# Kernel tuning notes

Measured on AMD Instinct MI355X. Metric: run time of the kernel, lower is better.

The kernel has to match this reference:

```python
import jax, jax.numpy as jnp
import numpy as np
from jax import lax

B, P, K = 16, 1024, 32          # clouds, points per cloud, kNN neighbors
N = B * P
NCLS = 40
DIMS = [3, 64, 128, 256]


def setup_inputs() -> dict:
    key = jax.random.key(0)
    ks = jax.random.split(key, 16)
    inp = {
        "x": jax.random.normal(ks[0], (N, DIMS[0]), dtype=jnp.float32),
        "batch": jnp.repeat(jnp.arange(B, dtype=jnp.int64), P),
        "target": jax.random.randint(ks[1], (N,), 0, NCLS, dtype=jnp.int64),
    }
    for i, (fi, fo) in enumerate(zip(DIMS[:-1], DIMS[1:])):
        scale = 1.0 / np.sqrt(2 * fi)
        inp[f"W{i+1}"] = jax.random.normal(ks[2 + 2 * i], (2 * fi, fo), dtype=jnp.float32) * scale
        inp[f"b{i+1}"] = jnp.zeros((fo,), dtype=jnp.float32)
    inp["Wc"] = jax.random.normal(ks[10], (DIMS[-1], NCLS), dtype=jnp.float32) * (1.0 / np.sqrt(DIMS[-1]))
    inp["bc"] = jnp.zeros((NCLS,), dtype=jnp.float32)
    return inp


def knn_graph(x):
    """Per-cloud kNN (loop=False). x: [N,F] with nodes grouped in B clouds of P.
    Returns global neighbor indices [N, K]."""
    xb = x.reshape(B, P, -1)
    sq = jnp.sum(xb * xb, axis=-1)                       # [B,P]
    d2 = sq[:, :, None] + sq[:, None, :] - 2.0 * jnp.einsum("bpf,bqf->bpq", xb, xb)
    d2 = d2 + jnp.eye(P, dtype=x.dtype) * jnp.finfo(x.dtype).max  # exclude self-loops
    _, idx = lax.top_k(-d2, K)                           # [B,P,K] local indices
    gidx = idx + (jnp.arange(B) * P)[:, None, None]      # local -> global node ids
    return gidx.reshape(N, K)


def edge_conv(x, nbr, W, b):
    """EdgeConv: max_j MLP([x_i, x_j - x_i])."""
    xj = x[nbr]                                          # [N,K,F] gather
    xi = x[:, None, :]
    feat = jnp.concatenate([jnp.broadcast_to(xi, xj.shape), xj - xi], axis=-1)  # [N,K,2F]
    h = jnp.einsum("nkf,fo->nko", feat, W) + b           # [N,K,F']
    return jnp.max(h, axis=1)                            # max aggregation


def reference(x, batch, target, W1, b1, W2, b2, W3, b3, Wc, bc):
    del batch  # structure encoded as B clouds of P contiguous nodes
    for W, b in ((W1, b1), (W2, b2), (W3, b3)):
        nbr = knn_graph(x)                               # dynamic graph per layer
        x = jax.nn.relu(edge_conv(x, nbr, W, b))
    logits = x @ Wc + bc                                 # [N, NCLS]
    probs = jax.nn.softmax(logits, axis=-1)
    logp = jax.nn.log_softmax(logits, axis=-1)           # == probs.log()
    loss = -jnp.mean(jnp.take_along_axis(logp, target[:, None], axis=-1))
    return loss, probs
```

## Files before the change

### kernel.cpp

```cpp
#include <hip/hip_runtime.h>
#include <float.h>
#include <math.h>

#define BCLOUDS 16
#define PPTS    1024
#define NPTS    (BCLOUDS * PPTS)
#define KNB     32
#define NCLS    40
#define RPB     4
#define NBIN    256
#define HPADW   (NBIN + NBIN / 16)
#define SELFM   0xFFFFFFFFu

__device__ __forceinline__ int hidx(int b) { return b + (b >> 4); }

template<int F>
__global__ __launch_bounds__(256) void xpose_kernel(const float* __restrict__ x,
                                                    float* __restrict__ xT,
                                                    float* __restrict__ qn) {
    const int p = blockIdx.x * 256 + threadIdx.x;
    const int cloud = p >> 10, pl = p & 1023;
    const float* xr = x + (size_t)p * F;
    float* xTc = xT + (size_t)cloud * F * PPTS;
    float s = 0.f;
    for (int f = 0; f < F; ++f) {
        const float v = xr[f];
        s = fmaf(v, v, s);
        xTc[(size_t)f * PPTS + pl] = v;
    }
    qn[p] = s;
}

template<int F>
__global__ __launch_bounds__(256, 6) void knn_kernel(const float* __restrict__ x,
                                                     const float* __restrict__ xT,
                                                     const float* __restrict__ qn,
                                                     int* __restrict__ nbr) {
    __shared__ unsigned dmat[RPB][PPTS];
    __shared__ float    xp[RPB][F];
    __shared__ float    rn[RPB];
    __shared__ unsigned hist[RPB][HPADW];

    const int tid   = threadIdx.x;
    const int lane  = tid & 63;
    const int wave  = tid >> 6;
    const int bid   = blockIdx.x;
    const int cloud = (bid & 7) + 8 * (bid >> 11);
    const int pl0   = ((bid >> 3) & 255) * RPB;

    const float* xc = x + (size_t)cloud * PPTS * F;
    for (int i = tid; i < RPB * F; i += 256)
        xp[i / F][i % F] = xc[(size_t)(pl0 + i / F) * F + (i % F)];
    __syncthreads();
    if (tid < RPB) {
        float s = 0.f;
        for (int f = 0; f < F; ++f) { const float v = xp[tid][f]; s = fmaf(v, v, s); }
        rn[tid] = s;
    }
    __syncthreads();

    const float* xTc = xT + (size_t)cloud * F * PPTS;
    const float4 qv = *reinterpret_cast<const float4*>(&qn[cloud * PPTS + 4 * tid]);

    float acc[RPB][4];
#pragma unroll
    for (int r = 0; r < RPB; ++r)
#pragma unroll
        for (int c = 0; c < 4; ++c) acc[r][c] = 0.f;

    if constexpr (F % 4 == 0) {
#pragma unroll 2
        for (int f4 = 0; f4 < F / 4; ++f4) {
            float4 vf[4];
#pragma unroll
            for (int j = 0; j < 4; ++j)
                vf[j] = *reinterpret_cast<const float4*>(&xTc[(size_t)(4 * f4 + j) * PPTS + 4 * tid]);
            float4 xr[RPB];
#pragma unroll
            for (int r = 0; r < RPB; ++r) xr[r] = *reinterpret_cast<const float4*>(&xp[r][4 * f4]);
#pragma unroll
            for (int r = 0; r < RPB; ++r) {
                acc[r][0] = fmaf(vf[0].x, xr[r].x, acc[r][0]);
                acc[r][1] = fmaf(vf[0].y, xr[r].x, acc[r][1]);
                acc[r][2] = fmaf(vf[0].z, xr[r].x, acc[r][2]);
                acc[r][3] = fmaf(vf[0].w, xr[r].x, acc[r][3]);
                acc[r][0] = fmaf(vf[1].x, xr[r].y, acc[r][0]);
                acc[r][1] = fmaf(vf[1].y, xr[r].y, acc[r][1]);
                acc[r][2] = fmaf(vf[1].z, xr[r].y, acc[r][2]);
                acc[r][3] = fmaf(vf[1].w, xr[r].y, acc[r][3]);
                acc[r][0] = fmaf(vf[2].x, xr[r].z, acc[r][0]);
                acc[r][1] = fmaf(vf[2].y, xr[r].z, acc[r][1]);
                acc[r][2] = fmaf(vf[2].z, xr[r].z, acc[r][2]);
                acc[r][3] = fmaf(vf[2].w, xr[r].z, acc[r][3]);
                acc[r][0] = fmaf(vf[3].x, xr[r].w, acc[r][0]);
                acc[r][1] = fmaf(vf[3].y, xr[r].w, acc[r][1]);
                acc[r][2] = fmaf(vf[3].z, xr[r].w, acc[r][2]);
                acc[r][3] = fmaf(vf[3].w, xr[r].w, acc[r][3]);
            }
        }
    } else {
        for (int f = 0; f < F; ++f) {
            const float4 v = *reinterpret_cast<const float4*>(&xTc[(size_t)f * PPTS + 4 * tid]);
#pragma unroll
            for (int r = 0; r < RPB; ++r) {
                const float xv = xp[r][f];
                acc[r][0] = fmaf(v.x, xv, acc[r][0]);
                acc[r][1] = fmaf(v.y, xv, acc[r][1]);
                acc[r][2] = fmaf(v.z, xv, acc[r][2]);
                acc[r][3] = fmaf(v.w, xv, acc[r][3]);
            }
        }
    }
#pragma unroll
    for (int r = 0; r < RPB; ++r) {
        uint4 wv;
        float d2;
        d2 = fmaxf(rn[r] + qv.x - 2.f * acc[r][0], 0.f);
        wv.x = (4 * tid + 0 == pl0 + r) ? SELFM : __float_as_uint(d2);
        d2 = fmaxf(rn[r] + qv.y - 2.f * acc[r][1], 0.f);
        wv.y = (4 * tid + 1 == pl0 + r) ? SELFM : __float_as_uint(d2);
        d2 = fmaxf(rn[r] + qv.z - 2.f * acc[r][2], 0.f);
        wv.z = (4 * tid + 2 == pl0 + r) ? SELFM : __float_as_uint(d2);
        d2 = fmaxf(rn[r] + qv.w - 2.f * acc[r][3], 0.f);
        wv.w = (4 * tid + 3 == pl0 + r) ? SELFM : __float_as_uint(d2);
        *reinterpret_cast<uint4*>(&dmat[r][4 * tid]) = wv;
    }
    __syncthreads();

    unsigned* hw = hist[wave];
    const int r = wave;
    unsigned bits[16];
#pragma unroll
    for (int i = 0; i < 16; ++i) bits[i] = dmat[r][lane + i * 64];

    unsigned m = bits[0];
#pragma unroll
    for (int i = 1; i < 16; ++i) m = min(m, bits[i]);
    unsigned gmin = m;
    unsigned tmax = (lane < 32) ? m : 0u;
#pragma unroll
    for (int off = 1; off < 64; off <<= 1) {
        gmin = min(gmin, (unsigned)__shfl_xor((int)gmin, off));
        tmax = max(tmax, (unsigned)__shfl_xor((int)tmax, off));
    }

    unsigned sm = 0u, nam = 0xFFFFu;
    int R = KNB;
    unsigned base = gmin;
    int shift = 0;
    bool do_hist = tmax > gmin;
    if (do_hist) {
        const unsigned span = tmax - gmin;
        const int lg = 31 - __clz(span);
        shift = lg > 7 ? lg - 7 : 0;
    }

#pragma unroll 1
    for (int pass = 0; pass < 2 && do_hist; ++pass) {
        int bin[16];
#pragma unroll
        for (int j = 0; j < 5; ++j) { const int k2 = lane + j * 64; if (k2 < HPADW) hw[k2] = 0u; }
#pragma unroll
        for (int i = 0; i < 16; ++i) {
            if ((nam >> i) & 1) {
                const unsigned d = bits[i] - base;
                int b = (int)(d >> shift);
                b = b > 255 ? 255 : b;
                bin[i] = b;
                atomicAdd(&hw[hidx(b)], 1u);
            } else bin[i] = 256;
        }
        unsigned h[4];
        int cnt = 0;
#pragma unroll
        for (int j = 0; j < 4; ++j) { h[j] = hw[hidx(lane * 4 + j)]; cnt += (int)h[j]; }
        int inc = cnt;
#pragma unroll
        for (int off = 1; off < 64; off <<= 1) {
            const int nv = __shfl_up(inc, off);
            if (lane >= off) inc += nv;
        }
        const int pre = inc - cnt;
        const bool found = (pre < R && R <= inc);
        unsigned pk = 0;
        if (found) {
            int c = pre, bb = -1, cb = 0; unsigned hbv = 0;
#pragma unroll
            for (int j = 0; j < 4; ++j) {
                if (bb < 0) {
                    if (c + (int)h[j] >= R) { bb = lane * 4 + j; hbv = h[j]; cb = c; }
                    else c += (int)h[j];
                }
            }
            pk = (unsigned)bb | ((unsigned)cb << 8) | (hbv << 16);
        }
        const unsigned long long fm = __ballot(found);
        pk = (unsigned)__shfl((int)pk, __ffsll(fm) - 1);
        const int bbin = (int)(pk & 255u);
        const int cb   = (int)((pk >> 8) & 255u);
        const int hb   = (int)(pk >> 16);
        const int need = R - cb;
        unsigned nnam = 0u;
#pragma unroll
        for (int i = 0; i < 16; ++i) {
            if (bin[i] < bbin) sm |= 1u << i;
            else if (bin[i] == bbin) nnam |= 1u << i;
        }
        if (hb == need && bbin != 255) {
            sm |= nnam; R = 0; do_hist = false;
        } else {
            nam = nnam; R = need;
            if (R <= 4 || shift == 0) do_hist = false;
            else {
                base += (unsigned)bbin << shift;
                shift = shift > 8 ? shift - 8 : 0;
            }
        }
    }

#pragma unroll 1
    while (R > 0) {
        unsigned lmin = 0xFFFFFFFFu;
#pragma unroll
        for (int i = 0; i < 16; ++i)
            if ((nam >> i) & 1) lmin = min(lmin, bits[i]);
        unsigned vmin = lmin;
#pragma unroll
        for (int off = 1; off < 64; off <<= 1)
            vmin = min(vmin, (unsigned)__shfl_xor((int)vmin, off));
        unsigned eq = 0u;
#pragma unroll
        for (int i = 0; i < 16; ++i)
            if (((nam >> i) & 1) && bits[i] == vmin) eq |= 1u << i;
        int tot = __popc(eq);
#pragma unroll
        for (int off = 1; off < 64; off <<= 1) tot += __shfl_xor(tot, off);
        if (tot <= R) {
            sm |= eq; nam &= ~eq; R -= tot;
        } else {
#pragma unroll
            for (int i = 0; i < 16; ++i) {
                if (R > 0) {
                    const bool c2 = (eq >> i) & 1;
                    const unsigned long long mb = __ballot(c2);
                    const int t2 = (int)__popcll(mb);
                    if (t2 <= R) { if (c2) sm |= 1u << i; R -= t2; }
                    else {
                        const unsigned long long lower = mb & ((1ull << lane) - 1ull);
                        if (c2 && (int)__popcll(lower) < R) sm |= 1u << i;
                        R = 0;
                    }
                }
            }
        }
    }

    int* out = nbr + (size_t)(cloud * PPTS + pl0 + r) * KNB;
    int tot = 0;
#pragma unroll
    for (int i = 0; i < 16; ++i) {
        const bool c2 = (sm >> i) & 1;
        const unsigned long long mb = __ballot(c2);
        if (c2) {
            const int slot = tot + (int)__popcll(mb & ((1ull << lane) - 1ull));
            if (slot < KNB) out[slot] = cloud * PPTS + lane + i * 64;
        }
        tot += (int)__popcll(mb);
    }
    if (lane == 0)
        for (int s = tot; s < KNB; ++s) out[s] = cloud * PPTS + pl0 + r;
}

template<int F, int FO>
__global__ __launch_bounds__(256) void edge_gemm_kernel(const float* __restrict__ x,
                                                        const float* __restrict__ W,
                                                        const float* __restrict__ bias,
                                                        float* __restrict__ A,
                                                        float* __restrict__ Bm) {
    constexpr int RT  = 16;
    constexpr int RS  = 256 / FO;
    constexpr int RPT = RT / RS;
    __shared__ float xs[RT][F];
    const int tid = threadIdx.x;
    const int n0  = blockIdx.x * RT;
    for (int i = tid; i < RT * F; i += 256)
        xs[i / F][i % F] = x[(size_t)n0 * F + i];
    __syncthreads();

    const int o  = tid % FO;
    const int r0 = tid / FO;
    float accA[RPT], accB[RPT];
#pragma unroll
    for (int i = 0; i < RPT; ++i) { accA[i] = 0.f; accB[i] = 0.f; }

    for (int f = 0; f < F; ++f) {
        const float wt = W[(size_t)f * FO + o];
        const float wb = W[(size_t)(F + f) * FO + o];
        const float wd = wt - wb;
#pragma unroll
        for (int i = 0; i < RPT; ++i) {
            const float xv = xs[r0 + i * RS][f];
            accA[i] = fmaf(xv, wd, accA[i]);
            accB[i] = fmaf(xv, wb, accB[i]);
        }
    }
    const float bo = bias[o];
#pragma unroll
    for (int i = 0; i < RPT; ++i) {
        const size_t row = (size_t)(n0 + r0 + i * RS);
        A[row * FO + o]  = accA[i] + bo;
        Bm[row * FO + o] = accB[i];
    }
}

template<int FO>
__global__ __launch_bounds__(256) void combine_kernel(const float* __restrict__ A,
                                                      const float* __restrict__ Bm,
                                                      const int* __restrict__ nbr,
                                                      float* __restrict__ xout) {
    constexpr int FO4 = FO / 4;
    const int bid = (int)((blockIdx.x & 7) * (gridDim.x >> 3) + (blockIdx.x >> 3));
    const int idx = bid * 256 + threadIdx.x;
    const int n  = idx / FO4;
    const int o4 = idx % FO4;
    const int* nb = nbr + (size_t)n * KNB;
    const float4* B4 = reinterpret_cast<const float4*>(Bm);
    float4 mx = make_float4(-FLT_MAX, -FLT_MAX, -FLT_MAX, -FLT_MAX);
#pragma unroll 8
    for (int k = 0; k < KNB; ++k) {
        const float4 v = B4[(size_t)nb[k] * FO4 + o4];
        mx.x = fmaxf(mx.x, v.x); mx.y = fmaxf(mx.y, v.y);
        mx.z = fmaxf(mx.z, v.z); mx.w = fmaxf(mx.w, v.w);
    }
    const float4 a = reinterpret_cast<const float4*>(A)[idx];
    float4 rr;
    rr.x = fmaxf(a.x + mx.x, 0.f);
    rr.y = fmaxf(a.y + mx.y, 0.f);
    rr.z = fmaxf(a.z + mx.z, 0.f);
    rr.w = fmaxf(a.w + mx.w, 0.f);
    reinterpret_cast<float4*>(xout)[idx] = rr;
}

__global__ __launch_bounds__(320) void cls_gemm_kernel(const float* __restrict__ x,
                                                       const float* __restrict__ Wc,
                                                       const float* __restrict__ bc,
                                                       float* __restrict__ logits) {
    constexpr int RT = 16;
    __shared__ float xs[RT][256];
    __shared__ float wsm[256][NCLS];
    const int tid = threadIdx.x;
    const int n0  = blockIdx.x * RT;

    const float4* xsrc = reinterpret_cast<const float4*>(x + (size_t)n0 * 256);
    float4* xdst = reinterpret_cast<float4*>(&xs[0][0]);
    for (int i = tid; i < RT * 256 / 4; i += 320) xdst[i] = xsrc[i];
    for (int i = tid; i < 256 * NCLS; i += 320) wsm[i / NCLS][i % NCLS] = Wc[i];
    __syncthreads();

    const int o  = tid % NCLS;
    const int rg = tid / NCLS;
    float acc0 = 0.f, acc1 = 0.f;
#pragma unroll 4
    for (int f4 = 0; f4 < 64; ++f4) {
        float wv0 = wsm[4 * f4 + 0][o];
        float wv1 = wsm[4 * f4 + 1][o];
        float wv2 = wsm[4 * f4 + 2][o];
        float wv3 = wsm[4 * f4 + 3][o];
        const float4 xa = *reinterpret_cast<const float4*>(&xs[rg][4 * f4]);
        const float4 xb = *reinterpret_cast<const float4*>(&xs[rg + 8][4 * f4]);
        acc0 = fmaf(xa.x, wv0, acc0); acc0 = fmaf(xa.y, wv1, acc0);
        acc0 = fmaf(xa.z, wv2, acc0); acc0 = fmaf(xa.w, wv3, acc0);
        acc1 = fmaf(xb.x, wv0, acc1); acc1 = fmaf(xb.y, wv1, acc1);
        acc1 = fmaf(xb.z, wv2, acc1); acc1 = fmaf(xb.w, wv3, acc1);
    }
    const float bo = bc[o];
    logits[(size_t)(n0 + rg) * NCLS + o]     = acc0 + bo;
    logits[(size_t)(n0 + rg + 8) * NCLS + o] = acc1 + bo;
}

__global__ __launch_bounds__(256) void softmax_loss_kernel(const float* __restrict__ logits,
                                                           const int* __restrict__ target,
                                                           float* __restrict__ probs,
                                                           float* __restrict__ lossbuf) {
    const int tid = threadIdx.x;
    const int lane = tid & 63;
    const int n = blockIdx.x * 4 + (tid >> 6);
    float logit = -FLT_MAX;
    if (lane < NCLS) logit = logits[(size_t)n * NCLS + lane];
    float m = logit;
#pragma unroll
    for (int off = 32; off; off >>= 1) m = fmaxf(m, __shfl_xor(m, off));
    const float e = (lane < NCLS) ? __expf(logit - m) : 0.f;
    float s = e;
#pragma unroll
    for (int off = 32; off; off >>= 1) s += __shfl_xor(s, off);
    if (lane < NCLS) probs[(size_t)n * NCLS + lane] = e / s;
    const float lt = __shfl(logit, target[n]);
    if (lane == 0) lossbuf[n] = logf(s) - (lt - m);
}

__global__ __launch_bounds__(256) void loss_reduce_kernel(const float* __restrict__ lossbuf,
                                                          float* __restrict__ out) {
    __shared__ float s[256];
    float acc = 0.f;
    for (int i = threadIdx.x; i < NPTS; i += 256) acc += lossbuf[i];
    s[threadIdx.x] = acc;
    __syncthreads();
    for (int off = 128; off; off >>= 1) {
        if (threadIdx.x < off) s[threadIdx.x] += s[threadIdx.x + off];
        __syncthreads();
    }
    if (threadIdx.x == 0) out[0] = s[0] / (float)NPTS;
}

extern "C" void kernel_launch(void* const* d_in, const int* in_sizes, int n_in,
                              void* d_out, int out_size, void* d_ws, size_t ws_size,
                              hipStream_t stream) {
    (void)in_sizes; (void)n_in; (void)out_size; (void)ws_size;
    const float* x_in   = (const float*)d_in[0];
    const int*   target = (const int*)d_in[2];
    const float* W1 = (const float*)d_in[3];
    const float* b1 = (const float*)d_in[4];
    const float* W2 = (const float*)d_in[5];
    const float* b2 = (const float*)d_in[6];
    const float* W3 = (const float*)d_in[7];
    const float* b3 = (const float*)d_in[8];
    const float* Wc = (const float*)d_in[9];
    const float* bc = (const float*)d_in[10];

    char* ws = (char*)d_ws;
    float* X       = (float*)(ws);
    float* A       = (float*)(ws + (size_t)16 * 1024 * 1024);
    float* Bm      = (float*)(ws + (size_t)32 * 1024 * 1024);
    float* xT      = (float*)(ws + (size_t)32 * 1024 * 1024);
    float* qn      = (float*)(ws + (size_t)40 * 1024 * 1024);
    int*   nbr     = (int*)  (ws + (size_t)48 * 1024 * 1024);
    float* lossbuf = (float*)(ws + (size_t)50 * 1024 * 1024);
    float* logits  = (float*)(ws + (size_t)16 * 1024 * 1024);

    float* outF  = (float*)d_out;
    float* probs = outF + 1;

    xpose_kernel<3><<<NPTS / 256, 256, 0, stream>>>(x_in, xT, qn);
    knn_kernel<3><<<NPTS / RPB, 256, 0, stream>>>(x_in, xT, qn, nbr);
    edge_gemm_kernel<3, 64><<<NPTS / 16, 256, 0, stream>>>(x_in, W1, b1, A, Bm);
    combine_kernel<64><<<NPTS * 16 / 256, 256, 0, stream>>>(A, Bm, nbr, X);

    xpose_kernel<64><<<NPTS / 256, 256, 0, stream>>>(X, xT, qn);
    knn_kernel<64><<<NPTS / RPB, 256, 0, stream>>>(X, xT, qn, nbr);
    edge_gemm_kernel<64, 128><<<NPTS / 16, 256, 0, stream>>>(X, W2, b2, A, Bm);
    combine_kernel<128><<<NPTS * 32 / 256, 256, 0, stream>>>(A, Bm, nbr, X);

    xpose_kernel<128><<<NPTS / 256, 256, 0, stream>>>(X, xT, qn);
    knn_kernel<128><<<NPTS / RPB, 256, 0, stream>>>(X, xT, qn, nbr);
    edge_gemm_kernel<128, 256><<<NPTS / 16, 256, 0, stream>>>(X, W3, b3, A, Bm);
    combine_kernel<256><<<NPTS * 64 / 256, 256, 0, stream>>>(A, Bm, nbr, X);

    cls_gemm_kernel<<<NPTS / 16, 320, 0, stream>>>(X, Wc, bc, logits);
    softmax_loss_kernel<<<NPTS / 4, 256, 0, stream>>>(logits, target, probs, lossbuf);
    loss_reduce_kernel<<<1, 256, 0, stream>>>(lossbuf, outF);
}
```

Measured before the change: 365.4 us.

## Process eight query rows per kNN block with two interleaved selections per wave

The kNN kernel now handles 8 query points per block instead of 4, so each loaded tile of transposed candidate features is reused across twice as many rows in the distance GEMM. Each wave runs two independent histogram radix-select passes interleaved for extra ILP. Bin indices are recomputed rather than stored to save registers. Occupancy hint drops from 6 to 3 blocks and shared memory roughly doubles. Fewer blocks and higher register pressure may hurt latency hiding.

```diff
diff --git a/kernel.cpp b/kernel.cpp
--- a/kernel.cpp
+++ b/kernel.cpp
@@ -7,7 +7,7 @@
 #define NPTS    (BCLOUDS * PPTS)
 #define KNB     32
 #define NCLS    40
-#define RPB     4
+#define RPB     8
 #define NBIN    256
 #define HPADW   (NBIN + NBIN / 16)
 #define SELFM   0xFFFFFFFFu
@@ -32,7 +32,7 @@
 }
 
 template<int F>
-__global__ __launch_bounds__(256, 6) void knn_kernel(const float* __restrict__ x,
+__global__ __launch_bounds__(256, 3) void knn_kernel(const float* __restrict__ x,
                                                      const float* __restrict__ xT,
                                                      const float* __restrict__ qn,
                                                      int* __restrict__ nbr) {
@@ -45,8 +45,8 @@
     const int lane  = tid & 63;
     const int wave  = tid >> 6;
     const int bid   = blockIdx.x;
-    const int cloud = (bid & 7) + 8 * (bid >> 11);
-    const int pl0   = ((bid >> 3) & 255) * RPB;
+    const int cloud = (bid & 7) + 8 * (bid >> 10);
+    const int pl0   = ((bid >> 3) & 127) * RPB;
 
     const float* xc = x + (size_t)cloud * PPTS * F;
     for (int i = tid; i < RPB * F; i += 256)
@@ -69,7 +69,7 @@
         for (int c = 0; c < 4; ++c) acc[r][c] = 0.f;
 
     if constexpr (F % 4 == 0) {
-#pragma unroll 2
+#pragma unroll 1
         for (int f4 = 0; f4 < F / 4; ++f4) {
             float4 vf[4];
 #pragma unroll
@@ -127,103 +127,161 @@
     }
     __syncthreads();
 
-    unsigned* hw = hist[wave];
-    const int r = wave;
-    unsigned bits[16];
-#pragma unroll
-    for (int i = 0; i < 16; ++i) bits[i] = dmat[r][lane + i * 64];
-
-    unsigned m = bits[0];
-#pragma unroll
-    for (int i = 1; i < 16; ++i) m = min(m, bits[i]);
-    unsigned gmin = m;
-    unsigned tmax = (lane < 32) ? m : 0u;
+    const int r0 = wave, r1 = wave + 4;
+    unsigned* hw0 = hist[r0];
+    unsigned* hw1 = hist[r1];
+    unsigned bits0[16], bits1[16];
+#pragma unroll
+    for (int i = 0; i < 16; ++i) {
+        bits0[i] = dmat[r0][lane + i * 64];
+        bits1[i] = dmat[r1][lane + i * 64];
+    }
+
+    unsigned m0 = bits0[0], m1 = bits1[0];
+#pragma unroll
+    for (int i = 1; i < 16; ++i) { m0 = min(m0, bits0[i]); m1 = min(m1, bits1[i]); }
+    unsigned gmin0 = m0, gmin1 = m1;
+    unsigned tmax0 = (lane < 32) ? m0 : 0u;
+    unsigned tmax1 = (lane < 32) ? m1 : 0u;
 #pragma unroll
     for (int off = 1; off < 64; off <<= 1) {
-        gmin = min(gmin, (unsigned)__shfl_xor((int)gmin, off));
-        tmax = max(tmax, (unsigned)__shfl_xor((int)tmax, off));
-    }
-
-    unsigned sm = 0u, nam = 0xFFFFu;
-    int R = KNB;
-    unsigned base = gmin;
-    int shift = 0;
-    bool do_hist = tmax > gmin;
-    if (do_hist) {
-        const unsigned span = tmax - gmin;
-        const int lg = 31 - __clz(span);
-        shift = lg > 7 ? lg - 7 : 0;
-    }
+        gmin0 = min(gmin0, (unsigned)__shfl_xor((int)gmin0, off));
+        gmin1 = min(gmin1, (unsigned)__shfl_xor((int)gmin1, off));
+        tmax0 = max(tmax0, (unsigned)__shfl_xor((int)tmax0, off));
+        tmax1 = max(tmax1, (unsigned)__shfl_xor((int)tmax1, off));
+    }
+
+    unsigned sm0 = 0u, nam0 = 0xFFFFu, sm1 = 0u, nam1 = 0xFFFFu;
+    int R0 = KNB, R1 = KNB;
+    unsigned base0 = gmin0, base1 = gmin1;
+    int shift0 = 0, shift1 = 0;
+    bool do0 = tmax0 > gmin0, do1 = tmax1 > gmin1;
+    if (do0) { const unsigned sp = tmax0 - gmin0; const int lg = 31 - __clz(sp); shift0 = lg > 7 ? lg - 7 : 0; }
+    if (do1) { const unsigned sp = tmax1 - gmin1; const int lg = 31 - __clz(sp); shift1 = lg > 7 ? lg - 7 : 0; }
 
 #pragma unroll 1
-    for (int pass = 0; pass < 2 && do_hist; ++pass) {
-        int bin[16];
-#pragma unroll
-        for (int j = 0; j < 5; ++j) { const int k2 = lane + j * 64; if (k2 < HPADW) hw[k2] = 0u; }
-#pragma unroll
-        for (int i = 0; i < 16; ++i) {
-            if ((nam >> i) & 1) {
-                const unsigned d = bits[i] - base;
-                int b = (int)(d >> shift);
-                b = b > 255 ? 255 : b;
-                bin[i] = b;
-                atomicAdd(&hw[hidx(b)], 1u);
-            } else bin[i] = 256;
-        }
-        unsigned h[4];
-        int cnt = 0;
-#pragma unroll
-        for (int j = 0; j < 4; ++j) { h[j] = hw[hidx(lane * 4 + j)]; cnt += (int)h[j]; }
-        int inc = cnt;
+    for (int pass = 0; pass < 2 && (do0 || do1); ++pass) {
+#pragma unroll
+        for (int j = 0; j < 5; ++j) {
+            const int k2 = lane + j * 64;
+            if (k2 < HPADW) { hw0[k2] = 0u; hw1[k2] = 0u; }
+        }
+        if (do0) {
+#pragma unroll
+            for (int i = 0; i < 16; ++i) {
+                if ((nam0 >> i) & 1) {
+                    int b = (int)((bits0[i] - base0) >> shift0);
+                    b = b > 255 ? 255 : b;
+                    atomicAdd(&hw0[hidx(b)], 1u);
+                }
+            }
+        }
+        if (do1) {
+#pragma unroll
+            for (int i = 0; i < 16; ++i) {
+                if ((nam1 >> i) & 1) {
+                    int b = (int)((bits1[i] - base1) >> shift1);
+                    b = b > 255 ? 255 : b;
+                    atomicAdd(&hw1[hidx(b)], 1u);
+                }
+            }
+        }
+        unsigned h0[4], h1[4];
+        int cnt0 = 0, cnt1 = 0;
+#pragma unroll
+        for (int j = 0; j < 4; ++j) {
+            h0[j] = hw0[hidx(lane * 4 + j)]; cnt0 += (int)h0[j];
+            h1[j] = hw1[hidx(lane * 4 + j)]; cnt1 += (int)h1[j];
+        }
+        int inc0 = cnt0, inc1 = cnt1;
 #pragma unroll
         for (int off = 1; off < 64; off <<= 1) {
-            const int nv = __shfl_up(inc, off);
-            if (lane >= off) inc += nv;
-        }
-        const int pre = inc - cnt;
-        const bool found = (pre < R && R <= inc);
-        unsigned pk = 0;
-        if (found) {
-            int c = pre, bb = -1, cb = 0; unsigned hbv = 0;
+            const int nv0 = __shfl_up(inc0, off);
+            const int nv1 = __shfl_up(inc1, off);
+            if (lane >= off) { inc0 += nv0; inc1 += nv1; }
+        }
+        const int pre0 = inc0 - cnt0, pre1 = inc1 - cnt1;
+        const bool found0 = do0 && (pre0 < R0 && R0 <= inc0);
+        const bool found1 = do1 && (pre1 < R1 && R1 <= inc1);
+        unsigned pk0 = 0, pk1 = 0;
+        if (found0) {
+            int c = pre0, bb = -1, cb = 0; unsigned hbv = 0;
 #pragma unroll
             for (int j = 0; j < 4; ++j) {
                 if (bb < 0) {
-                    if (c + (int)h[j] >= R) { bb = lane * 4 + j; hbv = h[j]; cb = c; }
-                    else c += (int)h[j];
-                }
-            }
-            pk = (unsigned)bb | ((unsigned)cb << 8) | (hbv << 16);
-        }
-        const unsigned long long fm = __ballot(found);
-        pk = (unsigned)__shfl((int)pk, __ffsll(fm) - 1);
-        const int bbin = (int)(pk & 255u);
-        const int cb   = (int)((pk >> 8) & 255u);
-        const int hb   = (int)(pk >> 16);
-        const int need = R - cb;
-        unsigned nnam = 0u;
-#pragma unroll
-        for (int i = 0; i < 16; ++i) {
-            if (bin[i] < bbin) sm |= 1u << i;
-            else if (bin[i] == bbin) nnam |= 1u << i;
-        }
-        if (hb == need && bbin != 255) {
-            sm |= nnam; R = 0; do_hist = false;
-        } else {
-            nam = nnam; R = need;
-            if (R <= 4 || shift == 0) do_hist = false;
+                    if (c + (int)h0[j] >= R0) { bb = lane * 4 + j; hbv = h0[j]; cb = c; }
+                    else c += (int)h0[j];
+                }
+            }
+            pk0 = (unsigned)bb | ((unsigned)cb << 8) | (hbv << 16);
+        }
+        if (found1) {
+            int c = pre1, bb = -1, cb = 0; unsigned hbv = 0;
+#pragma unroll
+            for (int j = 0; j < 4; ++j) {
+                if (bb < 0) {
+                    if (c + (int)h1[j] >= R1) { bb = lane * 4 + j; hbv = h1[j]; cb = c; }
+                    else c += (int)h1[j];
+                }
+            }
+            pk1 = (unsigned)bb | ((unsigned)cb << 8) | (hbv << 16);
+        }
+        const unsigned long long fm0 = __ballot(found0);
+        const unsigned long long fm1 = __ballot(found1);
+        pk0 = (unsigned)__shfl((int)pk0, __ffsll(fm0) - 1);
+        pk1 = (unsigned)__shfl((int)pk1, __ffsll(fm1) - 1);
+        if (do0) {
+            const int bbin = (int)(pk0 & 255u);
+            const int cb   = (int)((pk0 >> 8) & 255u);
+            const int hb   = (int)(pk0 >> 16);
+            const int need = R0 - cb;
+            unsigned nnam = 0u;
+#pragma unroll
+            for (int i = 0; i < 16; ++i) {
+                if ((nam0 >> i) & 1) {
+                    int b = (int)((bits0[i] - base0) >> shift0);
+                    b = b > 255 ? 255 : b;
+                    if (b < bbin) sm0 |= 1u << i;
+                    else if (b == bbin) nnam |= 1u << i;
+                }
+            }
+            if (hb == need && bbin != 255) { sm0 |= nnam; R0 = 0; do0 = false; }
             else {
-                base += (unsigned)bbin << shift;
-                shift = shift > 8 ? shift - 8 : 0;
+                nam0 = nnam; R0 = need;
+                if (R0 <= 4 || shift0 == 0) do0 = false;
+                else { base0 += (unsigned)bbin << shift0; shift0 = shift0 > 8 ? shift0 - 8 : 0; }
+            }
+        }
+        if (do1) {
+            const int bbin = (int)(pk1 & 255u);
+            const int cb   = (int)((pk1 >> 8) & 255u);
+            const int hb   = (int)(pk1 >> 16);
+            const int need = R1 - cb;
+            unsigned nnam = 0u;
+#pragma unroll
+            for (int i = 0; i < 16; ++i) {
+                if ((nam1 >> i) & 1) {
+                    int b = (int)((bits1[i] - base1) >> shift1);
+                    b = b > 255 ? 255 : b;
+                    if (b < bbin) sm1 |= 1u << i;
+                    else if (b == bbin) nnam |= 1u << i;
+                }
+            }
+            if (hb == need && bbin != 255) { sm1 |= nnam; R1 = 0; do1 = false; }
+            else {
+                nam1 = nnam; R1 = need;
+                if (R1 <= 4 || shift1 == 0) do1 = false;
+                else { base1 += (unsigned)bbin << shift1; shift1 = shift1 > 8 ? shift1 - 8 : 0; }
             }
         }
     }
 
 #pragma unroll 1
-    while (R > 0) {
+    while (R0 > 0) {
         unsigned lmin = 0xFFFFFFFFu;
 #pragma unroll
         for (int i = 0; i < 16; ++i)
-            if ((nam >> i) & 1) lmin = min(lmin, bits[i]);
+            if ((nam0 >> i) & 1) lmin = min(lmin, bits0[i]);
         unsigned vmin = lmin;
 #pragma unroll
         for (int off = 1; off < 64; off <<= 1)
@@ -231,44 +289,96 @@
         unsigned eq = 0u;
 #pragma unroll
         for (int i = 0; i < 16; ++i)
-            if (((nam >> i) & 1) && bits[i] == vmin) eq |= 1u << i;
+            if (((nam0 >> i) & 1) && bits0[i] == vmin) eq |= 1u << i;
         int tot = __popc(eq);
 #pragma unroll
         for (int off = 1; off < 64; off <<= 1) tot += __shfl_xor(tot, off);
-        if (tot <= R) {
-            sm |= eq; nam &= ~eq; R -= tot;
-        } else {
+        if (tot <= R0) { sm0 |= eq; nam0 &= ~eq; R0 -= tot; }
+        else {
 #pragma unroll
             for (int i = 0; i < 16; ++i) {
-                if (R > 0) {
+                if (R0 > 0) {
                     const bool c2 = (eq >> i) & 1;
                     const unsigned long long mb = __ballot(c2);
                     const int t2 = (int)__popcll(mb);
-                    if (t2 <= R) { if (c2) sm |= 1u << i; R -= t2; }
+                    if (t2 <= R0) { if (c2) sm0 |= 1u << i; R0 -= t2; }
                     else {
                         const unsigned long long lower = mb & ((1ull << lane) - 1ull);
-                        if (c2 && (int)__popcll(lower) < R) sm |= 1u << i;
-                        R = 0;
+                        if (c2 && (int)__popcll(lower) < R0) sm0 |= 1u << i;
+                        R0 = 0;
                     }
                 }
             }
         }
     }
-
-    int* out = nbr + (size_t)(cloud * PPTS + pl0 + r) * KNB;
-    int tot = 0;
-#pragma unroll
-    for (int i = 0; i < 16; ++i) {
-        const bool c2 = (sm >> i) & 1;
-        const unsigned long long mb = __ballot(c2);
-        if (c2) {
-            const int slot = tot + (int)__popcll(mb & ((1ull << lane) - 1ull));
-            if (slot < KNB) out[slot] = cloud * PPTS + lane + i * 64;
-        }
-        tot += (int)__popcll(mb);
-    }
-    if (lane == 0)
-        for (int s = tot; s < KNB; ++s) out[s] = cloud * PPTS + pl0 + r;
+#pragma unroll 1
+    while (R1 > 0) {
+        unsigned lmin = 0xFFFFFFFFu;
+#pragma unroll
+        for (int i = 0; i < 16; ++i)
+            if ((nam1 >> i) & 1) lmin = min(lmin, bits1[i]);
+        unsigned vmin = lmin;
+#pragma unroll
+        for (int off = 1; off < 64; off <<= 1)
+            vmin = min(vmin, (unsigned)__shfl_xor((int)vmin, off));
+        unsigned eq = 0u;
+#pragma unroll
+        for (int i = 0; i < 16; ++i)
+            if (((nam1 >> i) & 1) && bits1[i] == vmin) eq |= 1u << i;
+        int tot = __popc(eq);
+#pragma unroll
+        for (int off = 1; off < 64; off <<= 1) tot += __shfl_xor(tot, off);
+        if (tot <= R1) { sm1 |= eq; nam1 &= ~eq; R1 -= tot; }
+        else {
+#pragma unroll
+            for (int i = 0; i < 16; ++i) {
+                if (R1 > 0) {
+                    const bool c2 = (eq >> i) & 1;
+                    const unsigned long long mb = __ballot(c2);
+                    const int t2 = (int)__popcll(mb);
+                    if (t2 <= R1) { if (c2) sm1 |= 1u << i; R1 -= t2; }
+                    else {
+                        const unsigned long long lower = mb & ((1ull << lane) - 1ull);
+                        if (c2 && (int)__popcll(lower) < R1) sm1 |= 1u << i;
+                        R1 = 0;
+                    }
+                }
+            }
+        }
+    }
+
+    {
+        int* out = nbr + (size_t)(cloud * PPTS + pl0 + r0) * KNB;
+        int tot = 0;
+#pragma unroll
+        for (int i = 0; i < 16; ++i) {
+            const bool c2 = (sm0 >> i) & 1;
+            const unsigned long long mb = __ballot(c2);
+            if (c2) {
+                const int slot = tot + (int)__popcll(mb & ((1ull << lane) - 1ull));
+                if (slot < KNB) out[slot] = cloud * PPTS + lane + i * 64;
+            }
+            tot += (int)__popcll(mb);
+        }
+        if (lane == 0)
+            for (int s = tot; s < KNB; ++s) out[s] = cloud * PPTS + pl0 + r0;
+    }
+    {
+        int* out = nbr + (size_t)(cloud * PPTS + pl0 + r1) * KNB;
+        int tot = 0;
+#pragma unroll
+        for (int i = 0; i < 16; ++i) {
+            const bool c2 = (sm1 >> i) & 1;
+            const unsigned long long mb = __ballot(c2);
+            if (c2) {
+                const int slot = tot + (int)__popcll(mb & ((1ull << lane) - 1ull));
+                if (slot < KNB) out[slot] = cloud * PPTS + lane + i * 64;
+            }
+            tot += (int)__popcll(mb);
+        }
+        if (lane == 0)
+            for (int s = tot; s < KNB; ++s) out[s] = cloud * PPTS + pl0 + r1;
+    }
 }
 
 template<int F, int FO>
```

New measurement: 384.5 us. +5.2%, slower.
